# Optimization experiments

Hardware: AMD Instinct MI355X
Metric: run time of the kernel (lower is better)

The kernel has to match this reference:

```python
import jax, jax.numpy as jnp
import numpy as np

EMBED_DIM = 512
N_HEADS = 8
HEAD_DIM = EMBED_DIM // N_HEADS
MAX_H = 64
MAX_W = 48
B, H, W = 2, 64, 48


def setup_inputs() -> dict:
    key = jax.random.key(0)
    k1, k2, k3, k4, k5 = jax.random.split(key, 5)
    x = jax.random.normal(k1, (B, H, W, EMBED_DIM), dtype=jnp.float32)
    # Linear weights stored as [in, out] (torch stores [out, in]; math is x @ W_in_out)
    w_qkv = jax.random.normal(k2, (EMBED_DIM, 3 * EMBED_DIM), dtype=jnp.float32) * (EMBED_DIM ** -0.5)
    w_out = jax.random.normal(k3, (EMBED_DIM, EMBED_DIM), dtype=jnp.float32) * (EMBED_DIM ** -0.5)
    rel_row_tab = jax.random.normal(k4, (2 * MAX_H - 1, N_HEADS), dtype=jnp.float32) * 0.02
    rel_col_tab = jax.random.normal(k5, (2 * MAX_W - 1, N_HEADS), dtype=jnp.float32) * 0.02
    return {"x": x, "w_qkv": w_qkv, "w_out": w_out,
            "rel_row_tab": rel_row_tab, "rel_col_tab": rel_col_tab}


def _rel_bias(rel_row_tab, rel_col_tab, height, width):
    # 2D relative position bias: [n_heads, S, S]
    row_idx = jnp.repeat(jnp.arange(height), width)          # [S]
    col_idx = jnp.tile(jnp.arange(width), height)            # [S]
    rel_row = jnp.clip(row_idx[:, None] - row_idx[None, :] + MAX_H - 1, 0, 2 * MAX_H - 2)
    rel_col = jnp.clip(col_idx[:, None] - col_idx[None, :] + MAX_W - 1, 0, 2 * MAX_W - 2)
    bias = rel_row_tab[rel_row] + rel_col_tab[rel_col]       # [S, S, n_heads]
    return jnp.transpose(bias, (2, 0, 1))                    # [n_heads, S, S]


def reference(x, w_qkv, w_out, rel_row_tab, rel_col_tab):
    b, h, w, d = x.shape
    s = h * w
    x_flat = x.reshape(b, s, d)
    qkv = x_flat @ w_qkv                                     # [b, s, 3d]
    qkv = qkv.reshape(b, s, 3, N_HEADS, HEAD_DIM)
    qkv = jnp.transpose(qkv, (2, 0, 3, 1, 4))                # [3, b, nh, s, hd]
    q, k, v = qkv[0], qkv[1], qkv[2]
    scale = HEAD_DIM ** -0.5
    attn = jnp.einsum('bhqd,bhkd->bhqk', q, k) * scale       # [b, nh, s, s]
    attn = attn + _rel_bias(rel_row_tab, rel_col_tab, h, w)[None]
    attn = jax.nn.softmax(attn, axis=-1)
    out = jnp.einsum('bhqk,bhkd->bhqd', attn, v)             # [b, nh, s, hd]
    out = jnp.transpose(out, (0, 2, 1, 3)).reshape(b, s, d)
    out = out @ w_out
    return out.reshape(b, h, w, d)
```

## Files before the change

kernel.cpp:

```cpp
#include <hip/hip_runtime.h>
#include <hip/hip_bf16.h>

#define S_TOK 3072
#define NHEADS 8
#define KVT 12800

typedef __attribute__((ext_vector_type(8))) short short8;
typedef __attribute__((ext_vector_type(4))) float floatx4;
typedef __attribute__((ext_vector_type(4))) unsigned short ushortx4;

__device__ __forceinline__ unsigned short f2bf(float f) {
  union { float f; unsigned u; } v; v.f = f;
  unsigned r = v.u + 0x7fffu + ((v.u >> 16) & 1u);
  return (unsigned short)(r >> 16);
}
__device__ __forceinline__ float bf2f(unsigned short h) {
  union { unsigned u; float f; } v; v.u = (unsigned)h << 16;
  return v.f;
}
__device__ __forceinline__ unsigned pack2bf(float a, float b) {
  __hip_bfloat162 h = __float22bfloat162_rn(make_float2(a, b));
  union { __hip_bfloat162 h; unsigned u; } c; c.h = h;
  return c.u;
}
__device__ __forceinline__ void gload16(const void* g, void* l) {
  __builtin_amdgcn_global_load_lds(
      (const __attribute__((address_space(1))) unsigned int*)g,
      (__attribute__((address_space(3))) unsigned int*)l, 16, 0, 0);
}

__global__ __launch_bounds__(256) void ga_conv_all(
    const float* __restrict__ X, const float* __restrict__ Wq,
    const float* __restrict__ Wo, unsigned short* __restrict__ xh,
    unsigned short* __restrict__ xl, unsigned short* __restrict__ wqh,
    unsigned short* __restrict__ wql, unsigned short* __restrict__ woh,
    unsigned short* __restrict__ wol) {
  const int blk = blockIdx.x;
  const int t = threadIdx.x;
  if (blk < 1536) {
    const int c = blk * 256 + t;
    const int m = c >> 6;
    const int c8 = (c & 63) << 3;
    const float* src = X + (size_t)m * 512 + c8;
    float4 v0 = *(const float4*)src, v1 = *(const float4*)(src + 4);
    float vv[8] = {v0.x, v0.y, v0.z, v0.w, v1.x, v1.y, v1.z, v1.w};
    union { unsigned short s[8]; short8 v; } hh, ll;
#pragma unroll
    for (int e = 0; e < 8; ++e) {
      hh.s[e] = f2bf(vv[e]);
      ll.s[e] = f2bf(vv[e] - bf2f(hh.s[e]));
    }
    const size_t dst = (size_t)m * 512 + (c8 ^ ((m & 7) << 3));
    *(short8*)&xh[dst] = hh.v;
    *(short8*)&xl[dst] = ll.v;
    return;
  }
  const int wq = (blk < 1728);
  const int b2 = wq ? (blk - 1536) : (blk - 1728);
  const int N = wq ? 1536 : 512;
  const float* W = wq ? Wq : Wo;
  unsigned short* th = wq ? wqh : woh;
  unsigned short* tl = wq ? wql : wol;
  const int k0 = (b2 & 7) * 64, n0 = (b2 >> 3) * 64;
  __shared__ float Ts[64][65];
#pragma unroll
  for (int i = 0; i < 4; ++i) {
    const int r = (t >> 4) + i * 16, c4 = (t & 15) * 4;
    float4 v = *(const float4*)&W[(size_t)(k0 + r) * N + n0 + c4];
    Ts[r][c4] = v.x; Ts[r][c4 + 1] = v.y; Ts[r][c4 + 2] = v.z; Ts[r][c4 + 3] = v.w;
  }
  __syncthreads();
#pragma unroll
  for (int j = 0; j < 2; ++j) {
    const int chunk = t * 2 + j;
    const int nl = chunk >> 3, m8 = chunk & 7;
    const int n = n0 + nl;
    const int ks = (m8 * 8) ^ ((n & 7) << 3);
    union { unsigned short s[8]; short8 v; } hh, ll;
#pragma unroll
    for (int e = 0; e < 8; ++e) {
      float f = Ts[ks + e][nl];
      hh.s[e] = f2bf(f);
      ll.s[e] = f2bf(f - bf2f(hh.s[e]));
    }
    const size_t dst = (size_t)n * 512 + k0 + m8 * 8;
    *(short8*)&th[dst] = hh.v;
    *(short8*)&tl[dst] = ll.v;
  }
}

template <int BM, int BN>
__global__ __launch_bounds__(256, 2) void ga_mm3(
    const unsigned short* __restrict__ Ah, const unsigned short* __restrict__ Al,
    const unsigned short* __restrict__ Bh, const unsigned short* __restrict__ Bl,
    unsigned short* __restrict__ Qd, unsigned short* __restrict__ KV,
    unsigned short* __restrict__ Vd) {
  const int tid = threadIdx.x;
  const int w = tid >> 6, l = tid & 63;
  const int g = l >> 4, ln = l & 15;
  const int wm = w >> 1, wn = w & 1;
  const int wgid = blockIdx.x;
  const int jj = (wgid & 7) * 72 + (wgid >> 3);
  const int m0 = (jj % 48) * BM;
  const int n0 = (jj / 48) * BN;
  const bool full3 = (n0 >= 1024);
  constexpr int MI = BM / 32;
  constexpr int NI = BN / 32;
  __shared__ unsigned short Alds[2][BM * 64];
  __shared__ unsigned short Blds[2][BN * 64];
  floatx4 acc[MI][NI];
#pragma unroll
  for (int mi = 0; mi < MI; ++mi)
#pragma unroll
    for (int ni = 0; ni < NI; ++ni)
#pragma unroll
      for (int r = 0; r < 4; ++r) acc[mi][ni][r] = 0.f;

  for (int k0 = 0; k0 < 512; k0 += 64) {
    __syncthreads();
    {
      constexpr int PWA = (BM * 128) / 4096;
      constexpr int PWB = (BN * 128) / 4096;
      const char* ga_h = (const char*)(Ah + (size_t)m0 * 512 + k0);
      const char* ga_l = (const char*)(Al + (size_t)m0 * 512 + k0);
      const char* gb_h = (const char*)(Bh + (size_t)n0 * 512 + k0);
      const char* gb_l = (const char*)(Bl + (size_t)n0 * 512 + k0);
#pragma unroll
      for (int i = 0; i < PWA; ++i) {
        const int off = (w * PWA + i) * 1024;
        const int gb = ((off >> 7) + (l >> 3)) * 1024 + (l & 7) * 16;
        gload16(ga_h + gb, (char*)&Alds[0][0] + off);
        gload16(ga_l + gb, (char*)&Alds[1][0] + off);
      }
#pragma unroll
      for (int i = 0; i < PWB; ++i) {
        const int off = (w * PWB + i) * 1024;
        const int gb = ((off >> 7) + (l >> 3)) * 1024 + (l & 7) * 16;
        gload16(gb_h + gb, (char*)&Blds[0][0] + off);
        gload16(gb_l + gb, (char*)&Blds[1][0] + off);
      }
    }
    asm volatile("s_waitcnt vmcnt(0)" ::: "memory");
    __syncthreads();
#pragma unroll
    for (int kk = 0; kk < 64; kk += 32) {
      const int kbase = kk + g * 8;
      short8 ah[MI], al[MI], bh[NI], bl[NI];
#pragma unroll
      for (int mi = 0; mi < MI; ++mi) {
        const int row = wm * (BM / 2) + mi * 16 + ln;
        const int a = row * 64 + (kbase ^ ((row & 7) << 3));
        ah[mi] = *(const short8*)&Alds[0][a];
        al[mi] = *(const short8*)&Alds[1][a];
      }
#pragma unroll
      for (int ni = 0; ni < NI; ++ni) {
        const int row = wn * (BN / 2) + ni * 16 + ln;
        const int a = row * 64 + (kbase ^ ((row & 7) << 3));
        bh[ni] = *(const short8*)&Blds[0][a];
        bl[ni] = *(const short8*)&Blds[1][a];
      }
#pragma unroll
      for (int mi = 0; mi < MI; ++mi)
#pragma unroll
        for (int ni = 0; ni < NI; ++ni) {
          acc[mi][ni] = __builtin_amdgcn_mfma_f32_16x16x32_bf16(
              ah[mi], bh[ni], acc[mi][ni], 0, 0, 0);
          acc[mi][ni] = __builtin_amdgcn_mfma_f32_16x16x32_bf16(
              al[mi], bh[ni], acc[mi][ni], 0, 0, 0);
          if (full3)
            acc[mi][ni] = __builtin_amdgcn_mfma_f32_16x16x32_bf16(
                ah[mi], bl[ni], acc[mi][ni], 0, 0, 0);
        }
    }
  }
  const int b = m0 / S_TOK;
  const int s_base = (m0 % S_TOK) + wm * (BM / 2);
#pragma unroll
  for (int ni = 0; ni < NI; ++ni) {
    const int ng = n0 + wn * (BN / 2) + ni * 16;
    const int which = ng >> 9;
    const int h = (ng >> 6) & 7;
    const int d = (ng & 63) + ln;
    const int bh = b * 8 + h;
    const float qs = (which == 0) ? 0.18033688f : 1.0f;
    if (which == 1) {
      unsigned short* kp = KV + (size_t)bh * 32 * KVT;
#pragma unroll
      for (int mi = 0; mi < MI; ++mi)
#pragma unroll
        for (int r = 0; r < 4; ++r) {
          const int s = s_base + mi * 16 + g * 4 + r;
          const int tile = s / 96;
          const int r96 = s - tile * 96;
          kp[tile * KVT + r96 * 64 + (d ^ ((s & 7) << 3))] =
              f2bf(acc[mi][ni][r]);
        }
    } else {
      unsigned short* hp =
          (which == 0 ? Qd : Vd) + (size_t)bh * S_TOK * 64;
#pragma unroll
      for (int mi = 0; mi < MI; ++mi)
#pragma unroll
        for (int r = 0; r < 4; ++r) {
          const int s = s_base + mi * 16 + g * 4 + r;
          hp[(size_t)s * 64 + d] = f2bf(acc[mi][ni][r] * qs);
        }
    }
  }
}

__global__ __launch_bounds__(256) void ga_vtrans(
    const unsigned short* __restrict__ V, unsigned short* __restrict__ KV) {
  const int t = threadIdx.x;
  const int wgid = blockIdx.x;
  const int i = wgid >> 3;
  const int bh = (wgid & 7) * 2 + (i >> 5);
  const int tile = i & 31;
  __shared__ unsigned short Ts[96][72];
  const unsigned short* vp = V + ((size_t)bh * S_TOK + tile * 96) * 64;
#pragma unroll
  for (int it = 0; it < 3; ++it) {
    int c = it * 256 + t;
    int s = c >> 3, d8 = c & 7;
    short8 v = *(const short8*)&vp[(size_t)s * 64 + d8 * 8];
    *(short8*)&Ts[s][d8 * 8] = v;
  }
  __syncthreads();
  unsigned short* op = KV + ((size_t)bh * 32 + tile) * KVT + 6144;
#pragma unroll
  for (int it = 0; it < 4; ++it) {
    int c2 = it * 256 + t;
    if (c2 < 832) {
      const int d = c2 / 13;
      const int kc8 = (c2 - d * 13) * 8;
      short8 o;
      if (kc8 < 96) {
#pragma unroll
        for (int j = 0; j < 8; ++j) {
          const int p = kc8 + j;
          const int key =
              (p >> 5) * 32 + ((p >> 2) & 1) * 16 + ((p >> 3) & 3) * 4 + (p & 3);
          o[j] = (short)Ts[key][d];
        }
      } else {
#pragma unroll
        for (int j = 0; j < 8; ++j) o[j] = 0;
      }
      *(short8*)&op[d * 104 + kc8] = o;
    }
  }
}

__global__ __launch_bounds__(256) void ga_attn16(
    const unsigned short* __restrict__ Q, const unsigned short* __restrict__ KVg,
    const float* __restrict__ rowtab, const float* __restrict__ coltab,
    unsigned short* __restrict__ Opart, float* __restrict__ Lpart, int nsplit) {
  const int tid = threadIdx.x;
  const int w = tid >> 6;
  const int l = tid & 63;
  const int g = l >> 4;
  const int ln = l & 15;
  const int wgid = blockIdx.x;
  const int idx = wgid >> 3;
  const int bpb = 24 * nsplit;
  const int bh = ((wgid & 7) << 1) + idx / bpb;
  const int rem = idx % bpb;
  const int sp = rem / 24;
  const int qb = rem % 24;
  const int h = bh & 7;
  const int q0 = qb * 128 + w * 32;
  const int tiles_per_split = 32 / nsplit;

  __shared__ float rtab[127];
  __shared__ float ctab[95];
  __shared__ unsigned short KVlds[2][KVT];
  for (int i = tid; i < 127; i += 256) rtab[i] = rowtab[i * 8 + h] * 1.44269504f;
  for (int i = tid; i < 95; i += 256) ctab[i] = coltab[i * 8 + h] * 1.44269504f;

  const unsigned short* Qp = Q + (size_t)bh * S_TOK * 64;
  const unsigned short* KVp = KVg + (size_t)bh * 32 * KVT;

  const int t0 = sp * tiles_per_split;
  const int tend = t0 + tiles_per_split;

  auto STAGE = [&](int b, int t) {
    const char* src = (const char*)(KVp + (size_t)t * KVT);
    char* dst = (char*)&KVlds[b][0];
#pragma unroll
    for (int i = 0; i < 6; ++i)
      gload16(src + i * 4096 + tid * 16, dst + i * 4096 + tid * 16);
    if (tid < 64) gload16(src + 24576 + tid * 16, dst + 24576 + tid * 16);
  };

  STAGE(0, t0);
  asm volatile("s_waitcnt vmcnt(0)" ::: "memory");
  __syncthreads();

  int qr[2], qc[2];
  short8 qf[2][2];
  float ctr[2][3][4];
#pragma unroll
  for (int u = 0; u < 2; ++u) {
    const int q = q0 + u * 16 + ln;
    qr[u] = q / 48;
    qc[u] = q - qr[u] * 48;
    qf[u][0] = *(const short8*)&Qp[(size_t)q * 64 + g * 8];
    qf[u][1] = *(const short8*)&Qp[(size_t)q * 64 + 32 + g * 8];
    const float* cb = &ctab[qc[u] - g * 4 + 47];
#pragma unroll
    for (int m = 0; m < 3; ++m)
#pragma unroll
      for (int r = 0; r < 4; ++r) ctr[u][m][r] = cb[-(16 * m + r)];
  }

  short8 ones;
  {
    union { unsigned short s[8]; short8 v; } on;
#pragma unroll
    for (int j = 0; j < 8; ++j) on.s[j] = 0x3F80;
    ones = on.v;
  }

  floatx4 o_acc[2][4];
  floatx4 o5[2];
#pragma unroll
  for (int u = 0; u < 2; ++u) {
#pragma unroll
    for (int r = 0; r < 4; ++r) o5[u][r] = 0.f;
#pragma unroll
    for (int dt = 0; dt < 4; ++dt)
#pragma unroll
      for (int r = 0; r < 4; ++r) o_acc[u][dt][r] = 0.f;
  }

  int cur = 0;
  for (int t = t0; t < tend; ++t) {
    if (t + 1 < tend) STAGE(cur ^ 1, t + 1);
    const unsigned short* kb = &KVlds[cur][0];
    const unsigned short* vb = &KVlds[cur][6144];
    float rt[2][2];
#pragma unroll
    for (int u = 0; u < 2; ++u) {
      rt[u][0] = rtab[qr[u] + 63 - 2 * t] - 12.0f;
      rt[u][1] = rtab[qr[u] + 62 - 2 * t] - 12.0f;
    }
    const int swz = (ln & 7) << 3;
#pragma unroll
    for (int kc32 = 0; kc32 < 3; ++kc32) {
      float e[2][2][4];
#pragma unroll
      for (int kh = 0; kh < 2; ++kh) {
        const int kt = kc32 * 2 + kh;
        const int rb = (kt * 16 + ln) * 64;
        short8 kf0 = *(const short8*)&kb[rb + ((g * 8) ^ swz)];
        short8 kf1 = *(const short8*)&kb[rb + ((32 + g * 8) ^ swz)];
        const int m = kt % 3, wrap = kt / 3;
#pragma unroll
        for (int u = 0; u < 2; ++u) {
          floatx4 s;
#pragma unroll
          for (int r = 0; r < 4; ++r) s[r] = rt[u][wrap] + ctr[u][m][r];
          s = __builtin_amdgcn_mfma_f32_16x16x32_bf16(kf0, qf[u][0], s, 0, 0, 0);
          s = __builtin_amdgcn_mfma_f32_16x16x32_bf16(kf1, qf[u][1], s, 0, 0, 0);
#pragma unroll
          for (int r = 0; r < 4; ++r)
            e[u][kh][r] = __builtin_amdgcn_exp2f(s[r]);
        }
      }
      short8 pf[2];
#pragma unroll
      for (int u = 0; u < 2; ++u) {
        union { unsigned uu[4]; short8 v; } pk;
        pk.uu[0] = pack2bf(e[u][0][0], e[u][0][1]);
        pk.uu[1] = pack2bf(e[u][0][2], e[u][0][3]);
        pk.uu[2] = pack2bf(e[u][1][0], e[u][1][1]);
        pk.uu[3] = pack2bf(e[u][1][2], e[u][1][3]);
        pf[u] = pk.v;
      }
      __builtin_amdgcn_s_setprio(1);
#pragma unroll
      for (int dt = 0; dt < 4; ++dt) {
        const int vrow = dt * 16 + ln;
        short8 vf = *(const short8*)&vb[vrow * 104 + kc32 * 32 + g * 8];
        o_acc[0][dt] =
            __builtin_amdgcn_mfma_f32_16x16x32_bf16(pf[0], vf, o_acc[0][dt], 0, 0, 0);
        o_acc[1][dt] =
            __builtin_amdgcn_mfma_f32_16x16x32_bf16(pf[1], vf, o_acc[1][dt], 0, 0, 0);
      }
      o5[0] = __builtin_amdgcn_mfma_f32_16x16x32_bf16(pf[0], ones, o5[0], 0, 0, 0);
      o5[1] = __builtin_amdgcn_mfma_f32_16x16x32_bf16(pf[1], ones, o5[1], 0, 0, 0);
      __builtin_amdgcn_s_setprio(0);
    }
    asm volatile("s_waitcnt vmcnt(0)" ::: "memory");
    __syncthreads();
    cur ^= 1;
  }
  const size_t rowbase = (size_t)(sp * 16 + bh) * S_TOK;
#pragma unroll
  for (int u = 0; u < 2; ++u) {
    if (ln == 0) {
#pragma unroll
      for (int r = 0; r < 4; ++r)
        Lpart[rowbase + q0 + u * 16 + g * 4 + r] = o5[u][r];
    }
#pragma unroll
    for (int dt = 0; dt < 4; ++dt)
#pragma unroll
      for (int r = 0; r < 4; ++r)
        Opart[(rowbase + q0 + u * 16 + g * 4 + r) * 64 + dt * 16 + ln] =
            f2bf(o_acc[u][dt][r]);
  }
}

template <int NS>
__global__ __launch_bounds__(256, 2) void ga_outmm(
    const unsigned short* __restrict__ Opart, const float* __restrict__ Lpart,
    const unsigned short* __restrict__ Bh_, float* __restrict__ Out) {
  const int tid = threadIdx.x;
  const int w = tid >> 6, l = tid & 63;
  const int g = l >> 4, ln = l & 15;
  const int wm = w >> 1, wn = w & 1;
  const int m0 = blockIdx.x * 64;
  const int n0 = blockIdx.y * 64;
  __shared__ unsigned short Alds[64 * 64];
  __shared__ unsigned short Blds[2][64 * 64];
  floatx4 acc[2][2];
#pragma unroll
  for (int mi = 0; mi < 2; ++mi)
#pragma unroll
    for (int ni = 0; ni < 2; ++ni)
#pragma unroll
      for (int r = 0; r < 4; ++r) acc[mi][ni][r] = 0.f;

  const int lm = tid >> 2, lk4 = tid & 3;
  const int m = m0 + lm;
  const int b = (m >= S_TOK) ? 1 : 0;
  const int q = m - b * S_TOK;

  float v[16];
  float ls;
  auto ALOAD = [&](int h) {
    const int bh = b * 8 + h;
    ls = 0.f;
#pragma unroll
    for (int s = 0; s < NS; ++s) {
      const size_t row = (size_t)(s * 16 + bh) * S_TOK + q;
      ls += Lpart[row];
      const unsigned short* op = &Opart[row * 64 + lk4 * 16];
      short8 a0 = *(const short8*)op;
      short8 a1 = *(const short8*)(op + 8);
#pragma unroll
      for (int j = 0; j < 8; ++j) {
        float f0 = bf2f((unsigned short)a0[j]);
        float f1 = bf2f((unsigned short)a1[j]);
        if (s == 0) {
          v[j] = f0;
          v[8 + j] = f1;
        } else {
          v[j] += f0;
          v[8 + j] += f1;
        }
      }
    }
  };
  auto BISSUE = [&](int h, int buf) {
    const char* gb = (const char*)(Bh_ + (size_t)n0 * 512 + h * 64);
#pragma unroll
    for (int i = 0; i < 2; ++i) {
      const int off = (w * 2 + i) * 1024;
      const int gbo = ((off >> 7) + (l >> 3)) * 1024 + (l & 7) * 16;
      gload16(gb + gbo, (char*)&Blds[buf][0] + off);
    }
  };
  auto AWRITE = [&]() {
    const float inv = 1.0f / ls;
    unsigned pk[8];
#pragma unroll
    for (int j = 0; j < 8; ++j)
      pk[j] = pack2bf(v[2 * j] * inv, v[2 * j + 1] * inv);
    const int sw = (lm & 7) << 3;
    unsigned short* ab = &Alds[lm * 64];
#pragma unroll
    for (int j = 0; j < 4; ++j)
      *(uint2*)&ab[(lk4 * 16 + j * 4) ^ sw] = make_uint2(pk[2 * j], pk[2 * j + 1]);
  };

  ALOAD(0);
  BISSUE(0, 0);
  AWRITE();
  asm volatile("s_waitcnt vmcnt(0)" ::: "memory");
  __syncthreads();

  int cur = 0;
  for (int h = 0; h < 8; ++h) {
    if (h < 7) {
      ALOAD(h + 1);
      BISSUE(h + 1, cur ^ 1);
    }
#pragma unroll
    for (int kk = 0; kk < 64; kk += 32) {
      const int kbase = kk + g * 8;
      short8 af[2], bf[2];
#pragma unroll
      for (int mi = 0; mi < 2; ++mi) {
        const int row = wm * 32 + mi * 16 + ln;
        af[mi] = *(const short8*)&Alds[row * 64 + (kbase ^ ((row & 7) << 3))];
      }
#pragma unroll
      for (int ni = 0; ni < 2; ++ni) {
        const int row = wn * 32 + ni * 16 + ln;
        bf[ni] =
            *(const short8*)&Blds[cur][row * 64 + (kbase ^ ((row & 7) << 3))];
      }
#pragma unroll
      for (int mi = 0; mi < 2; ++mi)
#pragma unroll
        for (int ni = 0; ni < 2; ++ni)
          acc[mi][ni] = __builtin_amdgcn_mfma_f32_16x16x32_bf16(
              af[mi], bf[ni], acc[mi][ni], 0, 0, 0);
    }
    if (h < 7) {
      __syncthreads();
      AWRITE();
      __syncthreads();
      cur ^= 1;
    }
  }
#pragma unroll
  for (int mi = 0; mi < 2; ++mi)
#pragma unroll
    for (int ni = 0; ni < 2; ++ni)
#pragma unroll
      for (int r = 0; r < 4; ++r)
        Out[(size_t)(m0 + wm * 32 + mi * 16 + g * 4 + r) * 512 + n0 +
            wn * 32 + ni * 16 + ln] = acc[mi][ni][r];
}

extern "C" void kernel_launch(void* const* d_in, const int* in_sizes, int n_in,
                              void* d_out, int out_size, void* d_ws,
                              size_t ws_size, hipStream_t stream) {
  const float* x = (const float*)d_in[0];
  const float* w_qkv = (const float*)d_in[1];
  const float* w_out = (const float*)d_in[2];
  const float* rrow = (const float*)d_in[3];
  const float* rcol = (const float*)d_in[4];
  float* out = (float*)d_out;

  unsigned short* ws16 = (unsigned short*)d_ws;
  unsigned short* xh = ws16;
  unsigned short* xl = xh + 3145728;
  unsigned short* wqh = xl + 3145728;
  unsigned short* wql = wqh + 786432;
  unsigned short* woh = wql + 786432;
  unsigned short* wol = woh + 262144;
  unsigned short* Qb = wol + 262144;
  unsigned short* Vb = Qb + 3145728;
  unsigned short* KV = Vb + 3145728;
  unsigned short* Opart = KV + 6553600;
  const size_t base_bytes =
      ((size_t)3145728 * 4 + 786432 * 2 + 262144 * 2 + 6553600) * 2;
  const size_t per_split = (size_t)3145728 * 2 + (size_t)49152 * 4;
  const int nsplit = (ws_size >= base_bytes + 2 * per_split) ? 2 : 1;
  float* Lpart = (float*)(Opart + (size_t)nsplit * 3145728);

  ga_conv_all<<<1792, 256, 0, stream>>>(x, w_qkv, w_out, xh, xl, wqh, wql, woh,
                                        wol);
  ga_mm3<128, 128><<<576, 256, 0, stream>>>(xh, xl, wqh, wql, Qb, KV, Vb);
  ga_vtrans<<<512, 256, 0, stream>>>(Vb, KV);
  ga_attn16<<<24 * 16 * nsplit, 256, 0, stream>>>(
      Qb, KV, rrow, rcol, Opart, Lpart, nsplit);
  if (nsplit == 2)
    ga_outmm<2><<<dim3(96, 8), 256, 0, stream>>>(Opart, Lpart, woh, out);
  else
    ga_outmm<1><<<dim3(96, 8), 256, 0, stream>>>(Opart, Lpart, woh, out);
}
```

Measured before the change: 117.0 us.

## Fuse V transpose into QKV GEMM epilogue and swizzle out-proj block order

The QKV GEMM epilogue now writes V directly into the transposed, key-permuted layout inside the KV tile buffer. This removes the separate V transpose kernel and the intermediate V buffer round trip through memory. The output projection grid is flattened and remapped so that consecutive blocks spread across chiplets. One risk: the padding columns of the transposed V tiles are no longer zero-filled, which matters if the attention kernel reads them.

```diff
diff --git a/kernel.cpp b/kernel.cpp
--- a/kernel.cpp
+++ b/kernel.cpp
@@ -93,8 +93,7 @@
 __global__ __launch_bounds__(256, 2) void ga_mm3(
     const unsigned short* __restrict__ Ah, const unsigned short* __restrict__ Al,
     const unsigned short* __restrict__ Bh, const unsigned short* __restrict__ Bl,
-    unsigned short* __restrict__ Qd, unsigned short* __restrict__ KV,
-    unsigned short* __restrict__ Vd) {
+    unsigned short* __restrict__ Qd, unsigned short* __restrict__ KV) {
   const int tid = threadIdx.x;
   const int w = tid >> 6, l = tid & 63;
   const int g = l >> 4, ln = l & 15;
@@ -183,7 +182,6 @@
     const int h = (ng >> 6) & 7;
     const int d = (ng & 63) + ln;
     const int bh = b * 8 + h;
-    const float qs = (which == 0) ? 0.18033688f : 1.0f;
     if (which == 1) {
       unsigned short* kp = KV + (size_t)bh * 32 * KVT;
 #pragma unroll
@@ -196,58 +194,27 @@
           kp[tile * KVT + r96 * 64 + (d ^ ((s & 7) << 3))] =
               f2bf(acc[mi][ni][r]);
         }
+    } else if (which == 2) {
+      unsigned short* vt = KV + (size_t)bh * 32 * KVT + 6144;
+#pragma unroll
+      for (int mi = 0; mi < MI; ++mi) {
+        const int s0 = s_base + mi * 16 + g * 4;
+        const int tile = s0 / 96;
+        const int k96 = s0 - tile * 96;
+        const int pb = (k96 >> 5) * 32 + ((k96 >> 2) & 3) * 8 + ((k96 >> 4) & 1) * 4;
+        ushortx4 o = {f2bf(acc[mi][ni][0]), f2bf(acc[mi][ni][1]),
+                      f2bf(acc[mi][ni][2]), f2bf(acc[mi][ni][3])};
+        *(ushortx4*)&vt[(size_t)tile * KVT + d * 104 + pb] = o;
+      }
     } else {
-      unsigned short* hp =
-          (which == 0 ? Qd : Vd) + (size_t)bh * S_TOK * 64;
+      unsigned short* hp = Qd + (size_t)bh * S_TOK * 64;
 #pragma unroll
       for (int mi = 0; mi < MI; ++mi)
 #pragma unroll
         for (int r = 0; r < 4; ++r) {
           const int s = s_base + mi * 16 + g * 4 + r;
-          hp[(size_t)s * 64 + d] = f2bf(acc[mi][ni][r] * qs);
+          hp[(size_t)s * 64 + d] = f2bf(acc[mi][ni][r] * 0.18033688f);
         }
-    }
-  }
-}
-
-__global__ __launch_bounds__(256) void ga_vtrans(
-    const unsigned short* __restrict__ V, unsigned short* __restrict__ KV) {
-  const int t = threadIdx.x;
-  const int wgid = blockIdx.x;
-  const int i = wgid >> 3;
-  const int bh = (wgid & 7) * 2 + (i >> 5);
-  const int tile = i & 31;
-  __shared__ unsigned short Ts[96][72];
-  const unsigned short* vp = V + ((size_t)bh * S_TOK + tile * 96) * 64;
-#pragma unroll
-  for (int it = 0; it < 3; ++it) {
-    int c = it * 256 + t;
-    int s = c >> 3, d8 = c & 7;
-    short8 v = *(const short8*)&vp[(size_t)s * 64 + d8 * 8];
-    *(short8*)&Ts[s][d8 * 8] = v;
-  }
-  __syncthreads();
-  unsigned short* op = KV + ((size_t)bh * 32 + tile) * KVT + 6144;
-#pragma unroll
-  for (int it = 0; it < 4; ++it) {
-    int c2 = it * 256 + t;
-    if (c2 < 832) {
-      const int d = c2 / 13;
-      const int kc8 = (c2 - d * 13) * 8;
-      short8 o;
-      if (kc8 < 96) {
-#pragma unroll
-        for (int j = 0; j < 8; ++j) {
-          const int p = kc8 + j;
-          const int key =
-              (p >> 5) * 32 + ((p >> 2) & 1) * 16 + ((p >> 3) & 3) * 4 + (p & 3);
-          o[j] = (short)Ts[key][d];
-        }
-      } else {
-#pragma unroll
-        for (int j = 0; j < 8; ++j) o[j] = 0;
-      }
-      *(short8*)&op[d * 104 + kc8] = o;
     }
   }
 }
@@ -421,8 +388,10 @@
   const int w = tid >> 6, l = tid & 63;
   const int g = l >> 4, ln = l & 15;
   const int wm = w >> 1, wn = w & 1;
-  const int m0 = blockIdx.x * 64;
-  const int n0 = blockIdx.y * 64;
+  const int wgid = blockIdx.x;
+  const int i = wgid >> 3;
+  const int m0 = ((wgid & 7) * 12 + (i >> 3)) * 64;
+  const int n0 = (i & 7) * 64;
   __shared__ unsigned short Alds[64 * 64];
   __shared__ unsigned short Blds[2][64 * 64];
   floatx4 acc[2][2];
@@ -467,8 +436,8 @@
   auto BISSUE = [&](int h, int buf) {
     const char* gb = (const char*)(Bh_ + (size_t)n0 * 512 + h * 64);
 #pragma unroll
-    for (int i = 0; i < 2; ++i) {
-      const int off = (w * 2 + i) * 1024;
+    for (int i2 = 0; i2 < 2; ++i2) {
+      const int off = (w * 2 + i2) * 1024;
       const int gbo = ((off >> 7) + (l >> 3)) * 1024 + (l & 7) * 16;
       gload16(gb + gbo, (char*)&Blds[buf][0] + off);
     }
@@ -555,23 +524,21 @@
   unsigned short* woh = wql + 786432;
   unsigned short* wol = woh + 262144;
   unsigned short* Qb = wol + 262144;
-  unsigned short* Vb = Qb + 3145728;
-  unsigned short* KV = Vb + 3145728;
+  unsigned short* KV = Qb + 3145728;
   unsigned short* Opart = KV + 6553600;
   const size_t base_bytes =
-      ((size_t)3145728 * 4 + 786432 * 2 + 262144 * 2 + 6553600) * 2;
+      ((size_t)3145728 * 3 + 786432 * 2 + 262144 * 2 + 6553600) * 2;
   const size_t per_split = (size_t)3145728 * 2 + (size_t)49152 * 4;
   const int nsplit = (ws_size >= base_bytes + 2 * per_split) ? 2 : 1;
   float* Lpart = (float*)(Opart + (size_t)nsplit * 3145728);
 
   ga_conv_all<<<1792, 256, 0, stream>>>(x, w_qkv, w_out, xh, xl, wqh, wql, woh,
                                         wol);
-  ga_mm3<128, 128><<<576, 256, 0, stream>>>(xh, xl, wqh, wql, Qb, KV, Vb);
-  ga_vtrans<<<512, 256, 0, stream>>>(Vb, KV);
+  ga_mm3<128, 128><<<576, 256, 0, stream>>>(xh, xl, wqh, wql, Qb, KV);
   ga_attn16<<<24 * 16 * nsplit, 256, 0, stream>>>(
       Qb, KV, rrow, rcol, Opart, Lpart, nsplit);
   if (nsplit == 2)
-    ga_outmm<2><<<dim3(96, 8), 256, 0, stream>>>(Opart, Lpart, woh, out);
+    ga_outmm<2><<<768, 256, 0, stream>>>(Opart, Lpart, woh, out);
   else
-    ga_outmm<1><<<dim3(96, 8), 256, 0, stream>>>(Opart, Lpart, woh, out);
-}
+    ga_outmm<1><<<768, 256, 0, stream>>>(Opart, Lpart, woh, out);
+}
```

Result: no change. 115.2 us, median of 2 (-1.6%).
